# Kernel tuning notes

Hardware: AMD Instinct MI355X
Metric: run time of the kernel (lower is better)

The kernel has to match this reference:

```python
import jax, jax.numpy as jnp
import numpy as np

N = 100000      # nodes
E = 1600000     # edges
F_IN = 128      # node feature dim
F_E = 16        # edge feature dim
H = 4           # heads
C = 32          # per-head channels
NEG_SLOPE = 0.2


def setup_inputs() -> dict:
    key = jax.random.key(0)
    ks = jax.random.split(key, 8)
    s = 0.05
    x = jax.random.normal(ks[0], (N, F_IN), jnp.float32)
    edge_index = jax.random.randint(ks[1], (2, E), 0, N, jnp.int32)
    edge_attr = jax.random.normal(ks[2], (E, F_E), jnp.float32)
    Wl = jax.random.normal(ks[3], (F_IN, H * C), jnp.float32) * s   # lin_l (source)
    Wr = jax.random.normal(ks[4], (F_IN, H * C), jnp.float32) * s   # lin_r (target)
    We = jax.random.normal(ks[5], (F_E, H * C), jnp.float32) * s    # lin_edge
    att = jax.random.normal(ks[6], (H, C), jnp.float32) * s         # attention vector a
    bias = jnp.zeros((H * C,), jnp.float32)
    return {"x": x, "edge_index": edge_index, "edge_attr": edge_attr,
            "Wl": Wl, "Wr": Wr, "We": We, "att": att, "bias": bias}


def reference(x, edge_index, edge_attr, Wl, Wr, We, att, bias):
    n = x.shape[0]
    src, dst = edge_index[0], edge_index[1]

    # add_self_loops=True, fill_value='mean': self-loop edge_attr of node i is the
    # mean of edge_attr of edges whose destination is i (0 if no incoming edges).
    ea_sum = jax.ops.segment_sum(edge_attr, dst, num_segments=n)            # [n, Fe]
    cnt = jax.ops.segment_sum(jnp.ones((edge_attr.shape[0], 1), edge_attr.dtype),
                              dst, num_segments=n)                          # [n, 1]
    loop_attr = ea_sum / jnp.maximum(cnt, 1.0)
    loop = jnp.arange(n, dtype=src.dtype)
    src2 = jnp.concatenate([src, loop])                                     # [E+n]
    dst2 = jnp.concatenate([dst, loop])
    ea2 = jnp.concatenate([edge_attr, loop_attr], axis=0)                   # [E+n, Fe]

    # GATv2: score_e = att . leaky_relu(Wl x_src + Wr x_dst + We e)
    xl = (x @ Wl).reshape(n, H, C)
    xr = (x @ Wr).reshape(n, H, C)
    ee = (ea2 @ We).reshape(-1, H, C)
    e = jax.nn.leaky_relu(xl[src2] + xr[dst2] + ee, NEG_SLOPE)              # [E+n, H, C]
    logit = jnp.einsum('ehc,hc->eh', e, att)                                # [E+n, H]

    # segment softmax over destination node (self-loops guarantee nonempty segments)
    m = jax.ops.segment_max(logit, dst2, num_segments=n)                    # [n, H]
    ev = jnp.exp(logit - m[dst2])
    denom = jax.ops.segment_sum(ev, dst2, num_segments=n)
    alpha = ev / denom[dst2]                                                # [E+n, H]

    # scatter-aggregate weighted source messages
    out = jax.ops.segment_sum(alpha[:, :, None] * xl[src2], dst2, num_segments=n)
    out = out.reshape(n, H * C) + bias
    return jax.nn.relu(out), alpha
```

## Files before the change

kernel.cpp:

```cpp
#include <hip/hip_runtime.h>
#include <hip/hip_bf16.h>

#define HC   128
#define FE   16
#define NEG  0.2f
#define SPAD 140

using bf16 = __hip_bfloat16;
typedef short s16x8 __attribute__((ext_vector_type(8)));
typedef float f32x4 __attribute__((ext_vector_type(4)));

static __device__ __forceinline__ size_t szt(int a) { return (size_t)a; }
static __device__ __forceinline__ float bl(unsigned u) { return __uint_as_float(u << 16); }
static __device__ __forceinline__ float bh(unsigned u) { return __uint_as_float(u & 0xffff0000u); }
static __device__ __forceinline__ short b16rne(float f) {
    unsigned u = __float_as_uint(f);
    unsigned r = (u + 0x7fffu + ((u >> 16) & 1u)) >> 16;
    return (short)r;
}
static __device__ __forceinline__ unsigned pkbf(float x, float y) {
    return ((unsigned)(unsigned short)b16rne(y) << 16) | (unsigned)(unsigned short)b16rne(x);
}
static __device__ __forceinline__ int xcc_id() {
    int x;
    asm volatile("s_getreg_b32 %0, hwreg(HW_REG_XCC_ID)" : "=s"(x));
    return x & 7;
}


__global__ void k_rank(const int* __restrict__ dst, int* __restrict__ cnt2,
                       int* __restrict__ rank, int E) {
    int g = xcc_id();
    int base = (blockIdx.x * 256 + threadIdx.x) * 4;
    if (base >= E) return;
    unsigned gtag = (unsigned)g << 28;
    if (base + 3 < E) {
        int4 d4 = *reinterpret_cast<const int4*>(dst + base);
        int r0 = __hip_atomic_fetch_add(&cnt2[d4.x * 8 + g], 1, __ATOMIC_RELAXED,
                                        __HIP_MEMORY_SCOPE_WORKGROUP);
        int r1 = __hip_atomic_fetch_add(&cnt2[d4.y * 8 + g], 1, __ATOMIC_RELAXED,
                                        __HIP_MEMORY_SCOPE_WORKGROUP);
        int r2 = __hip_atomic_fetch_add(&cnt2[d4.z * 8 + g], 1, __ATOMIC_RELAXED,
                                        __HIP_MEMORY_SCOPE_WORKGROUP);
        int r3 = __hip_atomic_fetch_add(&cnt2[d4.w * 8 + g], 1, __ATOMIC_RELAXED,
                                        __HIP_MEMORY_SCOPE_WORKGROUP);
        *reinterpret_cast<int4*>(rank + base) =
            make_int4(r0 | gtag, r1 | gtag, r2 | gtag, r3 | gtag);
    } else {
        for (int e = base; e < E; ++e) {
            int r = __hip_atomic_fetch_add(&cnt2[dst[e] * 8 + g], 1, __ATOMIC_RELAXED,
                                           __HIP_MEMORY_SCOPE_WORKGROUP);
            rank[e] = r | gtag;
        }
    }
}

__global__ __launch_bounds__(1024) void k_scan1(const int* __restrict__ cnt,
                                                int* __restrict__ excl,
                                                int* __restrict__ bsum, int n) {
    __shared__ int wsum[16];
    int t = threadIdx.x, lane = t & 63, wv = t >> 6;
    int i = blockIdx.x * 4096 + t * 4;
    int4 c = make_int4(0, 0, 0, 0);
    if (i + 3 < n) c = *reinterpret_cast<const int4*>(&cnt[i]);
    else if (i < n) {
        c.x = cnt[i];
        c.y = (i + 1 < n) ? cnt[i + 1] : 0;
        c.z = (i + 2 < n) ? cnt[i + 2] : 0;
    }
    int tot = c.x + c.y + c.z + c.w;
    int s = tot;
    #pragma unroll
    for (int d = 1; d < 64; d <<= 1) { int u = __shfl_up(s, d); if (lane >= d) s += u; }
    if (lane == 63) wsum[wv] = s;
    __syncthreads();
    if (t < 16) {
        int ws = wsum[t];
        #pragma unroll
        for (int d = 1; d < 16; d <<= 1) { int u = __shfl_up(ws, d); if (t >= d) ws += u; }
        wsum[t] = ws;
    }
    __syncthreads();
    int excl_t = (wv ? wsum[wv - 1] : 0) + (s - tot);
    if (i < n) {
        int4 ro;
        ro.x = excl_t;
        ro.y = ro.x + c.x;
        ro.z = ro.y + c.y;
        ro.w = ro.z + c.z;
        if (i + 3 < n) *reinterpret_cast<int4*>(&excl[i]) = ro;
        else {
            excl[i] = ro.x;
            if (i + 1 < n) excl[i + 1] = ro.y;
            if (i + 2 < n) excl[i + 2] = ro.z;
        }
    }
    if (t == 0) bsum[blockIdx.x] = wsum[15];
}

__global__ void k_scan2(int* __restrict__ bsum, int nb) {
    int t = threadIdx.x;
    int carry = 0;
    for (int base = 0; base < nb; base += 64) {
        int i = base + t;
        int v = (i < nb) ? bsum[i] : 0;
        int s = v;
        #pragma unroll
        for (int d = 1; d < 64; d <<= 1) { int u = __shfl_up(s, d); if (t >= d) s += u; }
        if (i < nb) bsum[i] = carry + s - v;
        carry += __shfl(s, 63);
    }
}

__global__ void k_scan3(const int* __restrict__ bsum, int* __restrict__ off2,
                        int* __restrict__ row_off, int n8, int E) {
    int i = blockIdx.x * 256 + threadIdx.x;
    if (i < n8) {
        int v = off2[i] + bsum[i >> 12];
        off2[i] = v;
        if ((i & 7) == 0) row_off[i >> 3] = v;
    } else if (i == n8) {
        row_off[n8 >> 3] = E;
    }
}

__global__ void k_fill(const int* __restrict__ src, const int* __restrict__ dst,
                       const int* __restrict__ rank, const int* __restrict__ off2,
                       int4* __restrict__ pairs4, int E) {
    int base = (blockIdx.x * 256 + threadIdx.x) * 4;
    if (base >= E) return;
    if (base + 3 < E) {
        int4 d4 = *reinterpret_cast<const int4*>(dst + base);
        int4 s4 = *reinterpret_cast<const int4*>(src + base);
        int4 k4 = *reinterpret_cast<const int4*>(rank + base);
        int p0 = off2[d4.x * 8 + (((unsigned)k4.x) >> 28)] + (k4.x & 0x0FFFFFFF);
        int p1 = off2[d4.y * 8 + (((unsigned)k4.y) >> 28)] + (k4.y & 0x0FFFFFFF);
        int p2 = off2[d4.z * 8 + (((unsigned)k4.z) >> 28)] + (k4.z & 0x0FFFFFFF);
        int p3 = off2[d4.w * 8 + (((unsigned)k4.w) >> 28)] + (k4.w & 0x0FFFFFFF);
        pairs4[p0] = make_int4(s4.x, base + 0, d4.x, 0);
        pairs4[p1] = make_int4(s4.y, base + 1, d4.y, 0);
        pairs4[p2] = make_int4(s4.z, base + 2, d4.z, 0);
        pairs4[p3] = make_int4(s4.w, base + 3, d4.w, 0);
    } else {
        for (int e = base; e < E; ++e) {
            int d = dst[e], k = rank[e];
            int pos = off2[d * 8 + (((unsigned)k) >> 28)] + (k & 0x0FFFFFFF);
            pairs4[pos] = make_int4(src[e], e, d, 0);
        }
    }
}

__global__ void k_wprep(const float* __restrict__ Wl, const float* __restrict__ Wr,
                        s16x8* __restrict__ Wcf) {
    int idx = blockIdx.x * 256 + threadIdx.x;
    if (idx >= 4096) return;
    int kt = idx >> 10, nt = (idx >> 6) & 15, lane = idx & 63;
    int col = nt * 16 + (lane & 15);
    const float* W = (col < HC) ? Wl : Wr;
    int c = (col < HC) ? col : col - HC;
    s16x8 v;
    #pragma unroll
    for (int j = 0; j < 8; ++j) {
        int k = kt * 32 + (lane >> 4) * 8 + j;
        v[j] = b16rne(W[k * HC + c]);
    }
    Wcf[idx] = v;
}

__global__ void k_wprep2(const float* __restrict__ We, s16x8* __restrict__ Wecf) {
    int idx = blockIdx.x * 256 + threadIdx.x;
    if (idx >= 512) return;
    int lane = idx & 63, g = lane >> 4;
    int ch = (idx >> 6) * 16 + (lane & 15);
    s16x8 v = {0, 0, 0, 0, 0, 0, 0, 0};
    if (g < 2) {
        #pragma unroll
        for (int j = 0; j < 8; ++j)
            v[j] = b16rne(We[(g * 8 + j) * HC + ch]);
    }
    Wecf[idx] = v;
}


__global__ __launch_bounds__(256) void k_gemm2(const float* __restrict__ x,
                                               const s16x8* __restrict__ Wcf,
                                               bf16* __restrict__ xlb,
                                               bf16* __restrict__ xrb, int n) {
    int t = threadIdx.x, lane = t & 63, w = t >> 6;
    int m0 = blockIdx.x * 16;
    int arow = m0 + (lane & 15);
    if (arow >= n) arow = n - 1;
    const float* xrow = x + szt(arow) * HC + (lane >> 4) * 8;

    f32x4 acc[4];
    #pragma unroll
    for (int nt = 0; nt < 4; ++nt) acc[nt] = (f32x4){0.f, 0.f, 0.f, 0.f};

    #pragma unroll
    for (int kt = 0; kt < 4; ++kt) {
        float4 a0 = *reinterpret_cast<const float4*>(xrow + kt * 32);
        float4 a1 = *reinterpret_cast<const float4*>(xrow + kt * 32 + 4);
        s16x8 af;
        af[0] = b16rne(a0.x); af[1] = b16rne(a0.y);
        af[2] = b16rne(a0.z); af[3] = b16rne(a0.w);
        af[4] = b16rne(a1.x); af[5] = b16rne(a1.y);
        af[6] = b16rne(a1.z); af[7] = b16rne(a1.w);
        #pragma unroll
        for (int nt = 0; nt < 4; ++nt) {
            s16x8 bf = Wcf[(kt * 16 + w * 4 + nt) * 64 + lane];
            acc[nt] = __builtin_amdgcn_mfma_f32_16x16x32_bf16(af, bf, acc[nt], 0, 0, 0);
        }
    }

    bf16* O = (w < 2) ? xlb : xrb;
    int colb = (w & 1) * 64;
    #pragma unroll
    for (int nt = 0; nt < 4; ++nt) {
        int col = colb + nt * 16 + (lane & 15);
        #pragma unroll
        for (int q = 0; q < 4; ++q) {
            int r = m0 + (lane >> 4) * 4 + q;
            if (r < n) O[szt(r) * HC + col] = __float2bfloat16(acc[nt][q]);
        }
    }
}


__global__ __launch_bounds__(256) void k_self(
    const bf16* __restrict__ xlb, const bf16* __restrict__ xrb,
    const float* __restrict__ ea, const int4* __restrict__ pairs4,
    const int* __restrict__ row_off, const float* __restrict__ We,
    const float* __restrict__ att, float* __restrict__ exself, int n)
{
    int lane = threadIdx.x & 63, wv = threadIdx.x >> 6;
    int node = blockIdx.x * 4 + wv;
    if (node >= n) return;
    int beg = row_off[node], end = row_off[node + 1];
    int js = lane >> 3, f2 = (lane & 7) * 2;
    float sx = 0.f, sy = 0.f;
    if (beg < end) {
        int last = end - 1;
        int p = beg + js;
        int e_cur = pairs4[(p <= last) ? p : last].y;
        for (; p < end + js; p += 8) {
            int pn = p + 8; if (pn > last) pn = last;
            int e_next = pairs4[pn].y;
            float2 v = *reinterpret_cast<const float2*>(ea + szt(e_cur) * FE + f2);
            if (p < end) { sx += v.x; sy += v.y; }
            e_cur = e_next;
        }
    }
    sx += __shfl_xor(sx, 8);  sy += __shfl_xor(sy, 8);
    sx += __shfl_xor(sx, 16); sy += __shfl_xor(sy, 16);
    sx += __shfl_xor(sx, 32); sy += __shfl_xor(sy, 32);
    int deg = end - beg;
    float invd = (deg > 0) ? 1.f / (float)deg : 0.f;
    float mx = sx * invd, my = sy * invd;

    int c0 = lane * 2, h = lane >> 4;
    float e0 = 0.f, e1 = 0.f;
    #pragma unroll
    for (int kp = 0; kp < 8; ++kp) {
        float ae = __shfl(mx, kp);
        float ao = __shfl(my, kp);
        float2 we = *reinterpret_cast<const float2*>(We + (2 * kp) * HC + c0);
        float2 wo = *reinterpret_cast<const float2*>(We + (2 * kp + 1) * HC + c0);
        e0 += ae * we.x + ao * wo.x;
        e1 += ae * we.y + ao * wo.y;
    }
    unsigned xu = *reinterpret_cast<const unsigned*>(xlb + szt(node) * HC + c0);
    unsigned ru = *reinterpret_cast<const unsigned*>(xrb + szt(node) * HC + c0);
    float2 av = *reinterpret_cast<const float2*>(att + c0);
    float t0 = bl(xu) + bl(ru) + e0; t0 = t0 > 0.f ? t0 : NEG * t0;
    float t1 = bh(xu) + bh(ru) + e1; t1 = t1 > 0.f ? t1 : NEG * t1;
    float part = av.x * t0 + av.y * t1;
    part += __shfl_xor(part, 1);
    part += __shfl_xor(part, 2);
    part += __shfl_xor(part, 4);
    part += __shfl_xor(part, 8);
    float ex = __expf(part);
    if ((lane & 15) == 0) exself[szt(node) * 4 + h] = ex;
}


__global__ __launch_bounds__(256) void k_logit(
    const bf16* __restrict__ xlb, const bf16* __restrict__ xrb,
    const float* __restrict__ ea,
    const int4* __restrict__ pairs4,
    const s16x8* __restrict__ Wecf, const float* __restrict__ att,
    float* __restrict__ exe_csr, int E)
{
    __shared__ unsigned short sP[4][16][SPAD];
    int lane = threadIdx.x & 63, wv = threadIdx.x >> 6;
    int p0 = (blockIdx.x * 4 + wv) * 16;
    if (p0 >= E) return;
    unsigned short (*sPw)[SPAD] = sP[wv];

    int ei = lane & 15, g = lane >> 4;
    int p = p0 + ei; if (p >= E) p = E - 1;
    int4 pr = pairs4[p];

    s16x8 bfrag = {0, 0, 0, 0, 0, 0, 0, 0};
    if (g < 2) {
        const float* ear = ea + szt(pr.y) * FE + g * 8;
        float4 q0 = *reinterpret_cast<const float4*>(ear);
        float4 q1 = *reinterpret_cast<const float4*>(ear + 4);
        bfrag[0] = b16rne(q0.x); bfrag[1] = b16rne(q0.y);
        bfrag[2] = b16rne(q0.z); bfrag[3] = b16rne(q0.w);
        bfrag[4] = b16rne(q1.x); bfrag[5] = b16rne(q1.y);
        bfrag[6] = b16rne(q1.z); bfrag[7] = b16rne(q1.w);
    }
    #pragma unroll
    for (int mt = 0; mt < 8; ++mt) {
        f32x4 a = __builtin_amdgcn_mfma_f32_16x16x32_bf16(
            Wecf[mt * 64 + lane], bfrag, (f32x4){0.f, 0.f, 0.f, 0.f}, 0, 0, 0);
        *reinterpret_cast<uint2*>(&sPw[ei][mt * 16 + g * 4]) =
            make_uint2(pkbf(a[0], a[1]), pkbf(a[2], a[3]));
    }

    int l = lane & 15;
    int ch0 = l * 8;
    float4 av0 = *reinterpret_cast<const float4*>(att + ch0);
    float4 av1 = *reinterpret_cast<const float4*>(att + ch0 + 4);
    int m = E - p0; if (m > 16) m = 16;
    #pragma unroll
    for (int k = 0; k < 4; ++k) {
        int j = k * 4 + g;
        int sj = __shfl(pr.x, j);
        int dj = __shfl(pr.z, j);
        uint4 xv = *reinterpret_cast<const uint4*>(xlb + szt(sj) * HC + ch0);
        uint4 rv = *reinterpret_cast<const uint4*>(xrb + szt(dj) * HC + ch0);
        uint4 ev = *reinterpret_cast<const uint4*>(&sPw[j][ch0]);
        float t0 = bl(xv.x) + bl(rv.x) + bl(ev.x); t0 = t0 > 0.f ? t0 : NEG * t0;
        float t1 = bh(xv.x) + bh(rv.x) + bh(ev.x); t1 = t1 > 0.f ? t1 : NEG * t1;
        float t2 = bl(xv.y) + bl(rv.y) + bl(ev.y); t2 = t2 > 0.f ? t2 : NEG * t2;
        float t3 = bh(xv.y) + bh(rv.y) + bh(ev.y); t3 = t3 > 0.f ? t3 : NEG * t3;
        float t4 = bl(xv.z) + bl(rv.z) + bl(ev.z); t4 = t4 > 0.f ? t4 : NEG * t4;
        float t5 = bh(xv.z) + bh(rv.z) + bh(ev.z); t5 = t5 > 0.f ? t5 : NEG * t5;
        float t6 = bl(xv.w) + bl(rv.w) + bl(ev.w); t6 = t6 > 0.f ? t6 : NEG * t6;
        float t7 = bh(xv.w) + bh(rv.w) + bh(ev.w); t7 = t7 > 0.f ? t7 : NEG * t7;
        float part = av0.x * t0 + av0.y * t1 + av0.z * t2 + av0.w * t3
                   + av1.x * t4 + av1.y * t5 + av1.z * t6 + av1.w * t7;
        part += __shfl_xor(part, 1);
        part += __shfl_xor(part, 2);
        if ((lane & 3) == 0 && j < m)
            exe_csr[szt(p0 + j) * 4 + (l >> 2)] = __expf(part);
    }
}


__global__ __launch_bounds__(256) void k_aggr(
    const bf16* __restrict__ xlb, const float* __restrict__ exe_csr,
    const float* __restrict__ exself,
    const int4* __restrict__ pairs4, const int* __restrict__ row_off,
    const float* __restrict__ bias, float* __restrict__ out,
    float* __restrict__ alpha, int n, int E)
{
    int lane = threadIdx.x & 63, wv = threadIdx.x >> 6;
    int node = blockIdx.x * 4 + wv;
    if (node >= n) return;
    int j = lane >> 4, cg = lane & 15, cb = cg * 8, h = cg >> 2;
    int beg = row_off[node], end = row_off[node + 1];
    float acc[8];
    #pragma unroll
    for (int i = 0; i < 8; ++i) acc[i] = 0.f;
    float den = 0.f;

    if (beg < end) {
        int last = end - 1;
        int p0 = beg + j; if (p0 > last) p0 = last;
        int4 pr = pairs4[p0];
        float ex = exe_csr[szt(p0) * 4 + h];
        uint4 xv = *reinterpret_cast<const uint4*>(xlb + szt(pr.x) * HC + cb);
        for (int p = beg; p < end; p += 4) {
            int pn = p + 4 + j; if (pn > last) pn = last;
            int4 prN = pairs4[pn];
            float exN = exe_csr[szt(pn) * 4 + h];
            uint4 xvN = *reinterpret_cast<const uint4*>(xlb + szt(prN.x) * HC + cb);
            if (p + j < end) {
                den += ex;
                acc[0] += ex * bl(xv.x); acc[1] += ex * bh(xv.x);
                acc[2] += ex * bl(xv.y); acc[3] += ex * bh(xv.y);
                acc[4] += ex * bl(xv.z); acc[5] += ex * bh(xv.z);
                acc[6] += ex * bl(xv.w); acc[7] += ex * bh(xv.w);
            }
            pr = prN; ex = exN; xv = xvN;
        }
    }
    #pragma unroll
    for (int i = 0; i < 8; ++i) {
        acc[i] += __shfl_xor(acc[i], 16);
        acc[i] += __shfl_xor(acc[i], 32);
    }
    den += __shfl_xor(den, 16);
    den += __shfl_xor(den, 32);

    float exs = exself[szt(node) * 4 + h];
    uint4 xs = *reinterpret_cast<const uint4*>(xlb + szt(node) * HC + cb);
    den += exs;
    acc[0] += exs * bl(xs.x); acc[1] += exs * bh(xs.x);
    acc[2] += exs * bl(xs.y); acc[3] += exs * bh(xs.y);
    acc[4] += exs * bl(xs.z); acc[5] += exs * bh(xs.z);
    acc[6] += exs * bl(xs.w); acc[7] += exs * bh(xs.w);

    float inv = 1.f / den;
    if (j == 0) {
        float4 b0 = *reinterpret_cast<const float4*>(bias + cb);
        float4 b1 = *reinterpret_cast<const float4*>(bias + cb + 4);
        float4 o0, o1;
        o0.x = acc[0] * inv + b0.x; o0.x = o0.x > 0.f ? o0.x : 0.f;
        o0.y = acc[1] * inv + b0.y; o0.y = o0.y > 0.f ? o0.y : 0.f;
        o0.z = acc[2] * inv + b0.z; o0.z = o0.z > 0.f ? o0.z : 0.f;
        o0.w = acc[3] * inv + b0.w; o0.w = o0.w > 0.f ? o0.w : 0.f;
        o1.x = acc[4] * inv + b1.x; o1.x = o1.x > 0.f ? o1.x : 0.f;
        o1.y = acc[5] * inv + b1.y; o1.y = o1.y > 0.f ? o1.y : 0.f;
        o1.z = acc[6] * inv + b1.z; o1.z = o1.z > 0.f ? o1.z : 0.f;
        o1.w = acc[7] * inv + b1.w; o1.w = o1.w > 0.f ? o1.w : 0.f;
        *reinterpret_cast<float4*>(out + szt(node) * HC + cb) = o0;
        *reinterpret_cast<float4*>(out + szt(node) * HC + cb + 4) = o1;
        if ((cg & 3) == 0)
            alpha[szt(E + node) * 4 + h] = exs * inv;
    }
    float invh = __shfl(inv, 4 * (lane & 3));
    for (int pp = beg + (lane >> 2); pp < end; pp += 16) {
        int eid = pairs4[pp].y;
        alpha[szt(eid) * 4 + (lane & 3)] = exe_csr[szt(pp) * 4 + (lane & 3)] * invh;
    }
}


extern "C" void kernel_launch(void* const* d_in, const int* in_sizes, int n_in,
                              void* d_out, int out_size, void* d_ws, size_t ws_size,
                              hipStream_t stream) {
    const float* x    = (const float*)d_in[0];
    const int*   ei   = (const int*)d_in[1];
    const float* ea   = (const float*)d_in[2];
    const float* Wl   = (const float*)d_in[3];
    const float* Wr   = (const float*)d_in[4];
    const float* We   = (const float*)d_in[5];
    const float* att  = (const float*)d_in[6];
    const float* bias = (const float*)d_in[7];

    const int n = in_sizes[0] / HC;
    const int E = in_sizes[1] / 2;
    const int* src = ei;
    const int* dst = ei + E;
    const int n8 = n * 8;

    char* w = (char*)d_ws;
    size_t off = 0;
    auto alloc = [&](size_t bytes) -> char* {
        char* p = w + off;
        off += (bytes + 255) & ~(size_t)255;
        return p;
    };
    bf16*  xlb     = (bf16*) alloc((size_t)n * HC * 2);
    bf16*  xrb     = (bf16*) alloc((size_t)n * HC * 2);
    float* exe_csr = (float*)alloc((size_t)E * 4 * 4);
    float* exself  = (float*)alloc((size_t)n * 4 * 4);
    int*   cnt2    = (int*)  alloc((size_t)n8 * 4);
    int*   off2    = (int*)  alloc((size_t)n8 * 4);
    int*   row_off = (int*)  alloc((size_t)(n + 1) * 4);
    int*   rank    = (int*)  alloc((size_t)E * 4);
    int4*  pairs4  = (int4*) alloc((size_t)E * 16);
    s16x8* Wcf     = (s16x8*)alloc((size_t)4096 * 16);
    s16x8* Wecf    = (s16x8*)alloc((size_t)512 * 16);
    int    nb      = (n8 + 4095) / 4096;
    int*   bsum    = (int*)  alloc((size_t)nb * 4);
    (void)ws_size;

    float* out_p   = (float*)d_out;
    float* alpha_p = (float*)d_out + (size_t)n * HC;

    (void)hipMemsetAsync(cnt2, 0, (size_t)n8 * 4, stream);
    k_rank <<<(E / 4 + 255) / 256, 256, 0, stream>>>(dst, cnt2, rank, E);
    k_scan1<<<nb, 1024, 0, stream>>>(cnt2, off2, bsum, n8);
    k_scan2<<<1, 64, 0, stream>>>(bsum, nb);
    k_scan3<<<(n8 + 1 + 255) / 256, 256, 0, stream>>>(bsum, off2, row_off, n8, E);
    k_fill <<<(E / 4 + 255) / 256, 256, 0, stream>>>(src, dst, rank, off2, pairs4, E);
    k_wprep<<<16, 256, 0, stream>>>(Wl, Wr, Wcf);
    k_wprep2<<<2, 256, 0, stream>>>(We, Wecf);
    k_gemm2<<<(n + 15) / 16, 256, 0, stream>>>(x, Wcf, xlb, xrb, n);
    k_self <<<(n + 3) / 4, 256, 0, stream>>>(xlb, xrb, ea, pairs4, row_off, We, att,
                                             exself, n);
    k_logit<<<(E + 63) / 64, 256, 0, stream>>>(xlb, xrb, ea, pairs4,
                                               Wecf, att, exe_csr, E);
    k_aggr <<<(n + 3) / 4, 256, 0, stream>>>(xlb, exe_csr, exself, pairs4, row_off,
                                             bias, out_p, alpha_p, n, E);
}
```

Baseline: 468.9 us.

## Compute edge logits in original edge order and normalize alpha in separate pass

The logit kernel now walks edges in their original order, reading edge_attr contiguously and src/dst directly instead of gathering through the CSR permutation. The aggregation kernel reads exp-scores by edge id through the pairs array and stores per-node inverse denominators. A new kernel then writes alpha coalesced in edge order, replacing the scattered alpha writes done in the aggregation kernel. This trades random reads in the logit and alpha stages for a random exe gather in aggregation plus an extra pass over E.

New measurement: 497.8 us. 6.2% more time.

```diff
diff --git a/kernel.cpp b/kernel.cpp
--- a/kernel.cpp
+++ b/kernel.cpp
@@ -150,6 +150,7 @@
     }
 }
 
+
 __global__ void k_wprep(const float* __restrict__ Wl, const float* __restrict__ Wr,
                         s16x8* __restrict__ Wcf) {
     int idx = blockIdx.x * 256 + threadIdx.x;
@@ -286,23 +287,22 @@
 __global__ __launch_bounds__(256) void k_logit(
     const bf16* __restrict__ xlb, const bf16* __restrict__ xrb,
     const float* __restrict__ ea,
-    const int4* __restrict__ pairs4,
+    const int* __restrict__ src, const int* __restrict__ dst,
     const s16x8* __restrict__ Wecf, const float* __restrict__ att,
-    float* __restrict__ exe_csr, int E)
+    float* __restrict__ exe, int E)
 {
     __shared__ unsigned short sP[4][16][SPAD];
     int lane = threadIdx.x & 63, wv = threadIdx.x >> 6;
-    int p0 = (blockIdx.x * 4 + wv) * 16;
-    if (p0 >= E) return;
+    int e0 = (blockIdx.x * 4 + wv) * 16;
+    if (e0 >= E) return;
     unsigned short (*sPw)[SPAD] = sP[wv];
 
     int ei = lane & 15, g = lane >> 4;
-    int p = p0 + ei; if (p >= E) p = E - 1;
-    int4 pr = pairs4[p];
+    int e = e0 + ei; if (e >= E) e = E - 1;
 
     s16x8 bfrag = {0, 0, 0, 0, 0, 0, 0, 0};
     if (g < 2) {
-        const float* ear = ea + szt(pr.y) * FE + g * 8;
+        const float* ear = ea + szt(e) * FE + g * 8;
         float4 q0 = *reinterpret_cast<const float4*>(ear);
         float4 q1 = *reinterpret_cast<const float4*>(ear + 4);
         bfrag[0] = b16rne(q0.x); bfrag[1] = b16rne(q0.y);
@@ -322,12 +322,13 @@
     int ch0 = l * 8;
     float4 av0 = *reinterpret_cast<const float4*>(att + ch0);
     float4 av1 = *reinterpret_cast<const float4*>(att + ch0 + 4);
-    int m = E - p0; if (m > 16) m = 16;
+    int m = E - e0; if (m > 16) m = 16;
     #pragma unroll
     for (int k = 0; k < 4; ++k) {
         int j = k * 4 + g;
-        int sj = __shfl(pr.x, j);
-        int dj = __shfl(pr.z, j);
+        int ej = e0 + j; if (ej >= E) ej = E - 1;
+        int sj = src[ej];
+        int dj = dst[ej];
         uint4 xv = *reinterpret_cast<const uint4*>(xlb + szt(sj) * HC + ch0);
         uint4 rv = *reinterpret_cast<const uint4*>(xrb + szt(dj) * HC + ch0);
         uint4 ev = *reinterpret_cast<const uint4*>(&sPw[j][ch0]);
@@ -344,17 +345,17 @@
         part += __shfl_xor(part, 1);
         part += __shfl_xor(part, 2);
         if ((lane & 3) == 0 && j < m)
-            exe_csr[szt(p0 + j) * 4 + (l >> 2)] = __expf(part);
+            exe[szt(e0 + j) * 4 + (l >> 2)] = __expf(part);
     }
 }
 
 
 __global__ __launch_bounds__(256) void k_aggr(
-    const bf16* __restrict__ xlb, const float* __restrict__ exe_csr,
+    const bf16* __restrict__ xlb, const float* __restrict__ exe,
     const float* __restrict__ exself,
     const int4* __restrict__ pairs4, const int* __restrict__ row_off,
     const float* __restrict__ bias, float* __restrict__ out,
-    float* __restrict__ alpha, int n, int E)
+    float* __restrict__ alpha, float* __restrict__ invden, int n, int E)
 {
     int lane = threadIdx.x & 63, wv = threadIdx.x >> 6;
     int node = blockIdx.x * 4 + wv;
@@ -370,12 +371,12 @@
         int last = end - 1;
         int p0 = beg + j; if (p0 > last) p0 = last;
         int4 pr = pairs4[p0];
-        float ex = exe_csr[szt(p0) * 4 + h];
+        float ex = exe[szt(pr.y) * 4 + h];
         uint4 xv = *reinterpret_cast<const uint4*>(xlb + szt(pr.x) * HC + cb);
         for (int p = beg; p < end; p += 4) {
             int pn = p + 4 + j; if (pn > last) pn = last;
             int4 prN = pairs4[pn];
-            float exN = exe_csr[szt(pn) * 4 + h];
+            float exN = exe[szt(prN.y) * 4 + h];
             uint4 xvN = *reinterpret_cast<const uint4*>(xlb + szt(prN.x) * HC + cb);
             if (p + j < end) {
                 den += ex;
@@ -418,14 +419,23 @@
         o1.w = acc[7] * inv + b1.w; o1.w = o1.w > 0.f ? o1.w : 0.f;
         *reinterpret_cast<float4*>(out + szt(node) * HC + cb) = o0;
         *reinterpret_cast<float4*>(out + szt(node) * HC + cb + 4) = o1;
-        if ((cg & 3) == 0)
+        if ((cg & 3) == 0) {
             alpha[szt(E + node) * 4 + h] = exs * inv;
-    }
-    float invh = __shfl(inv, 4 * (lane & 3));
-    for (int pp = beg + (lane >> 2); pp < end; pp += 16) {
-        int eid = pairs4[pp].y;
-        alpha[szt(eid) * 4 + (lane & 3)] = exe_csr[szt(pp) * 4 + (lane & 3)] * invh;
-    }
+            invden[szt(node) * 4 + h] = inv;
+        }
+    }
+}
+
+
+__global__ void k_norm(const int* __restrict__ dst, const float* __restrict__ invden,
+                       const float* __restrict__ exe, float* __restrict__ alpha, int E) {
+    int e = blockIdx.x * 256 + threadIdx.x;
+    if (e >= E) return;
+    int d = dst[e];
+    float4 a  = *reinterpret_cast<const float4*>(exe + szt(e) * 4);
+    float4 iv = *reinterpret_cast<const float4*>(invden + szt(d) * 4);
+    a.x *= iv.x; a.y *= iv.y; a.z *= iv.z; a.w *= iv.w;
+    *reinterpret_cast<float4*>(alpha + szt(e) * 4) = a;
 }
 
 
@@ -456,8 +466,9 @@
     };
     bf16*  xlb     = (bf16*) alloc((size_t)n * HC * 2);
     bf16*  xrb     = (bf16*) alloc((size_t)n * HC * 2);
-    float* exe_csr = (float*)alloc((size_t)E * 4 * 4);
+    float* exe     = (float*)alloc((size_t)E * 4 * 4);
     float* exself  = (float*)alloc((size_t)n * 4 * 4);
+    float* invden  = (float*)alloc((size_t)n * 4 * 4);
     int*   cnt2    = (int*)  alloc((size_t)n8 * 4);
     int*   off2    = (int*)  alloc((size_t)n8 * 4);
     int*   row_off = (int*)  alloc((size_t)(n + 1) * 4);
@@ -481,10 +492,11 @@
     k_wprep<<<16, 256, 0, stream>>>(Wl, Wr, Wcf);
     k_wprep2<<<2, 256, 0, stream>>>(We, Wecf);
     k_gemm2<<<(n + 15) / 16, 256, 0, stream>>>(x, Wcf, xlb, xrb, n);
+    k_logit<<<(E + 63) / 64, 256, 0, stream>>>(xlb, xrb, ea, src, dst,
+                                               Wecf, att, exe, E);
     k_self <<<(n + 3) / 4, 256, 0, stream>>>(xlb, xrb, ea, pairs4, row_off, We, att,
                                              exself, n);
-    k_logit<<<(E + 63) / 64, 256, 0, stream>>>(xlb, xrb, ea, pairs4,
-                                               Wecf, att, exe_csr, E);
-    k_aggr <<<(n + 3) / 4, 256, 0, stream>>>(xlb, exe_csr, exself, pairs4, row_off,
-                                             bias, out_p, alpha_p, n, E);
-}
+    k_aggr <<<(n + 3) / 4, 256, 0, stream>>>(xlb, exe, exself, pairs4, row_off,
+                                             bias, out_p, alpha_p, invden, n, E);
+    k_norm <<<(E + 255) / 256, 256, 0, stream>>>(dst, invden, exe, alpha_p, E);
+}
```

## Permute edge attributes into CSR order as bf16 during fill

Applied to the files above, without the earlier changes.

During the CSR fill, each edge's 16 fp32 attributes are converted to bf16 and written at the edge's sorted position, giving a compact CSR-ordered copy. k_self and k_logit then read this copy contiguously instead of gathering fp32 rows through the original edge id. This removes the indirection and random gathers and halves the bytes read in the two consumers. In exchange, k_fill now does scattered 32-byte writes and drops its int4-vectorized loads, and the self-loop mean is taken over bf16-rounded values, which slightly changes precision.

After: 507.5 us. 8.2% more time.

```diff
diff --git a/kernel.cpp b/kernel.cpp
--- a/kernel.cpp
+++ b/kernel.cpp
@@ -126,29 +126,32 @@
 
 __global__ void k_fill(const int* __restrict__ src, const int* __restrict__ dst,
                        const int* __restrict__ rank, const int* __restrict__ off2,
-                       int4* __restrict__ pairs4, int E) {
+                       const float4* __restrict__ ea_in,
+                       int4* __restrict__ pairs4, uint4* __restrict__ eab, int E) {
     int base = (blockIdx.x * 256 + threadIdx.x) * 4;
     if (base >= E) return;
-    if (base + 3 < E) {
-        int4 d4 = *reinterpret_cast<const int4*>(dst + base);
-        int4 s4 = *reinterpret_cast<const int4*>(src + base);
-        int4 k4 = *reinterpret_cast<const int4*>(rank + base);
-        int p0 = off2[d4.x * 8 + (((unsigned)k4.x) >> 28)] + (k4.x & 0x0FFFFFFF);
-        int p1 = off2[d4.y * 8 + (((unsigned)k4.y) >> 28)] + (k4.y & 0x0FFFFFFF);
-        int p2 = off2[d4.z * 8 + (((unsigned)k4.z) >> 28)] + (k4.z & 0x0FFFFFFF);
-        int p3 = off2[d4.w * 8 + (((unsigned)k4.w) >> 28)] + (k4.w & 0x0FFFFFFF);
-        pairs4[p0] = make_int4(s4.x, base + 0, d4.x, 0);
-        pairs4[p1] = make_int4(s4.y, base + 1, d4.y, 0);
-        pairs4[p2] = make_int4(s4.z, base + 2, d4.z, 0);
-        pairs4[p3] = make_int4(s4.w, base + 3, d4.w, 0);
-    } else {
-        for (int e = base; e < E; ++e) {
+    #pragma unroll
+    for (int u = 0; u < 4; ++u) {
+        int e = base + u;
+        if (e < E) {
             int d = dst[e], k = rank[e];
             int pos = off2[d * 8 + (((unsigned)k) >> 28)] + (k & 0x0FFFFFFF);
             pairs4[pos] = make_int4(src[e], e, d, 0);
-        }
-    }
-}
+            float4 q0 = ea_in[szt(e) * 4 + 0];
+            float4 q1 = ea_in[szt(e) * 4 + 1];
+            float4 q2 = ea_in[szt(e) * 4 + 2];
+            float4 q3 = ea_in[szt(e) * 4 + 3];
+            uint4 lo, hi;
+            lo.x = pkbf(q0.x, q0.y); lo.y = pkbf(q0.z, q0.w);
+            lo.z = pkbf(q1.x, q1.y); lo.w = pkbf(q1.z, q1.w);
+            hi.x = pkbf(q2.x, q2.y); hi.y = pkbf(q2.z, q2.w);
+            hi.z = pkbf(q3.x, q3.y); hi.w = pkbf(q3.z, q3.w);
+            eab[szt(pos) * 2 + 0] = lo;
+            eab[szt(pos) * 2 + 1] = hi;
+        }
+    }
+}
+
 
 __global__ void k_wprep(const float* __restrict__ Wl, const float* __restrict__ Wr,
                         s16x8* __restrict__ Wcf) {
@@ -228,7 +231,7 @@
 
 __global__ __launch_bounds__(256) void k_self(
     const bf16* __restrict__ xlb, const bf16* __restrict__ xrb,
-    const float* __restrict__ ea, const int4* __restrict__ pairs4,
+    const unsigned* __restrict__ eab_u,
     const int* __restrict__ row_off, const float* __restrict__ We,
     const float* __restrict__ att, float* __restrict__ exself, int n)
 {
@@ -236,19 +239,11 @@
     int node = blockIdx.x * 4 + wv;
     if (node >= n) return;
     int beg = row_off[node], end = row_off[node + 1];
-    int js = lane >> 3, f2 = (lane & 7) * 2;
+    int js = lane >> 3, kp = lane & 7;
     float sx = 0.f, sy = 0.f;
-    if (beg < end) {
-        int last = end - 1;
-        int p = beg + js;
-        int e_cur = pairs4[(p <= last) ? p : last].y;
-        for (; p < end + js; p += 8) {
-            int pn = p + 8; if (pn > last) pn = last;
-            int e_next = pairs4[pn].y;
-            float2 v = *reinterpret_cast<const float2*>(ea + szt(e_cur) * FE + f2);
-            if (p < end) { sx += v.x; sy += v.y; }
-            e_cur = e_next;
-        }
+    for (int p = beg + js; p < end; p += 8) {
+        unsigned u = eab_u[szt(p) * 8 + kp];
+        sx += bl(u); sy += bh(u);
     }
     sx += __shfl_xor(sx, 8);  sy += __shfl_xor(sy, 8);
     sx += __shfl_xor(sx, 16); sy += __shfl_xor(sy, 16);
@@ -260,11 +255,11 @@
     int c0 = lane * 2, h = lane >> 4;
     float e0 = 0.f, e1 = 0.f;
     #pragma unroll
-    for (int kp = 0; kp < 8; ++kp) {
-        float ae = __shfl(mx, kp);
-        float ao = __shfl(my, kp);
-        float2 we = *reinterpret_cast<const float2*>(We + (2 * kp) * HC + c0);
-        float2 wo = *reinterpret_cast<const float2*>(We + (2 * kp + 1) * HC + c0);
+    for (int q = 0; q < 8; ++q) {
+        float ae = __shfl(mx, q);
+        float ao = __shfl(my, q);
+        float2 we = *reinterpret_cast<const float2*>(We + (2 * q) * HC + c0);
+        float2 wo = *reinterpret_cast<const float2*>(We + (2 * q + 1) * HC + c0);
         e0 += ae * we.x + ao * wo.x;
         e1 += ae * we.y + ao * wo.y;
     }
@@ -285,7 +280,7 @@
 
 __global__ __launch_bounds__(256) void k_logit(
     const bf16* __restrict__ xlb, const bf16* __restrict__ xrb,
-    const float* __restrict__ ea,
+    const uint4* __restrict__ eab,
     const int4* __restrict__ pairs4,
     const s16x8* __restrict__ Wecf, const float* __restrict__ att,
     float* __restrict__ exe_csr, int E)
@@ -301,15 +296,8 @@
     int4 pr = pairs4[p];
 
     s16x8 bfrag = {0, 0, 0, 0, 0, 0, 0, 0};
-    if (g < 2) {
-        const float* ear = ea + szt(pr.y) * FE + g * 8;
-        float4 q0 = *reinterpret_cast<const float4*>(ear);
-        float4 q1 = *reinterpret_cast<const float4*>(ear + 4);
-        bfrag[0] = b16rne(q0.x); bfrag[1] = b16rne(q0.y);
-        bfrag[2] = b16rne(q0.z); bfrag[3] = b16rne(q0.w);
-        bfrag[4] = b16rne(q1.x); bfrag[5] = b16rne(q1.y);
-        bfrag[6] = b16rne(q1.z); bfrag[7] = b16rne(q1.w);
-    }
+    if (g < 2)
+        bfrag = __builtin_bit_cast(s16x8, eab[szt(p) * 2 + g]);
     #pragma unroll
     for (int mt = 0; mt < 8; ++mt) {
         f32x4 a = __builtin_amdgcn_mfma_f32_16x16x32_bf16(
@@ -463,6 +451,7 @@
     int*   row_off = (int*)  alloc((size_t)(n + 1) * 4);
     int*   rank    = (int*)  alloc((size_t)E * 4);
     int4*  pairs4  = (int4*) alloc((size_t)E * 16);
+    uint4* eab     = (uint4*)alloc((size_t)E * 32);
     s16x8* Wcf     = (s16x8*)alloc((size_t)4096 * 16);
     s16x8* Wecf    = (s16x8*)alloc((size_t)512 * 16);
     int    nb      = (n8 + 4095) / 4096;
@@ -477,13 +466,14 @@
     k_scan1<<<nb, 1024, 0, stream>>>(cnt2, off2, bsum, n8);
     k_scan2<<<1, 64, 0, stream>>>(bsum, nb);
     k_scan3<<<(n8 + 1 + 255) / 256, 256, 0, stream>>>(bsum, off2, row_off, n8, E);
-    k_fill <<<(E / 4 + 255) / 256, 256, 0, stream>>>(src, dst, rank, off2, pairs4, E);
+    k_fill <<<(E / 4 + 255) / 256, 256, 0, stream>>>(src, dst, rank, off2,
+                                                     (const float4*)ea, pairs4, eab, E);
     k_wprep<<<16, 256, 0, stream>>>(Wl, Wr, Wcf);
     k_wprep2<<<2, 256, 0, stream>>>(We, Wecf);
     k_gemm2<<<(n + 15) / 16, 256, 0, stream>>>(x, Wcf, xlb, xrb, n);
-    k_self <<<(n + 3) / 4, 256, 0, stream>>>(xlb, xrb, ea, pairs4, row_off, We, att,
-                                             exself, n);
-    k_logit<<<(E + 63) / 64, 256, 0, stream>>>(xlb, xrb, ea, pairs4,
+    k_self <<<(n + 3) / 4, 256, 0, stream>>>(xlb, xrb, (const unsigned*)eab, row_off,
+                                             We, att, exself, n);
+    k_logit<<<(E + 63) / 64, 256, 0, stream>>>(xlb, xrb, eab, pairs4,
                                                Wecf, att, exe_csr, E);
     k_aggr <<<(n + 3) / 4, 256, 0, stream>>>(xlb, exe_csr, exself, pairs4, row_off,
                                              bias, out_p, alpha_p, n, E);
```
